# Kernel tuning notes

Measured on AMD Instinct MI355X. Metric: run time of the kernel, lower is better.

Reference implementation:

```python
import jax, jax.numpy as jnp
import numpy as np

DIM = 1024
NUM_HEADS = 16
HD = DIM // NUM_HEADS  # 64
ROPE_DIM = 64
ROPE_BASE = 10000.0


def setup_inputs() -> dict:
    key = jax.random.key(0)
    ks = jax.random.split(key, 5)
    B, N = 2, 2048
    s = 0.02
    return {
        "x": jax.random.normal(ks[0], (B, N, DIM), dtype=jnp.float32),
        "qkv_w": jax.random.normal(ks[1], (3 * DIM, DIM), dtype=jnp.float32) * s,
        "qkv_b": jax.random.normal(ks[2], (3 * DIM,), dtype=jnp.float32) * s,
        "proj_w": jax.random.normal(ks[3], (DIM, DIM), dtype=jnp.float32) * s,
        "proj_b": jax.random.normal(ks[4], (DIM,), dtype=jnp.float32) * s,
    }


def _apply_rope(t):
    # t: [B, H, N, D] with D even; interleaved (even, odd) pair rotation
    D = t.shape[-1]
    N = t.shape[2]
    pos = jnp.arange(N, dtype=t.dtype)
    inv = 1.0 / (ROPE_BASE ** (jnp.arange(0, D, 2, dtype=t.dtype) / D))
    freqs = pos[:, None] * inv[None, :]          # [N, D/2]
    cos = jnp.cos(freqs)[None, None]             # [1,1,N,D/2]
    sin = jnp.sin(freqs)[None, None]
    e = t[..., 0::2]
    o = t[..., 1::2]
    eo = e * cos - o * sin
    oo = e * sin + o * cos
    return jnp.stack([eo, oo], axis=-1).reshape(t.shape)


def reference(x, qkv_w, qkv_b, proj_w, proj_b):
    B, N, C = x.shape
    H, D = NUM_HEADS, HD
    scale = D ** -0.5
    qkv = x @ qkv_w.T + qkv_b                     # [B,N,3C]
    qkv = qkv.reshape(B, N, 3, H, D).transpose(2, 0, 3, 1, 4)  # [3,B,H,N,D]
    q, k, v = qkv[0], qkv[1], qkv[2]
    # RoPE on first ROPE_DIM dims of each head (here ROPE_DIM == HD)
    q = jnp.concatenate([_apply_rope(q[..., :ROPE_DIM]), q[..., ROPE_DIM:]], axis=-1)
    k = jnp.concatenate([_apply_rope(k[..., :ROPE_DIM]), k[..., ROPE_DIM:]], axis=-1)
    attn = jnp.einsum('bhnd,bhmd->bhnm', q, k) * scale
    attn = jax.nn.softmax(attn, axis=-1)
    out = jnp.einsum('bhnm,bhmd->bhnd', attn, v)  # [B,H,N,D]
    out = out.transpose(0, 2, 1, 3).reshape(B, N, C)
    return out @ proj_w.T + proj_b
```

## Files before the change

### kernel.cpp

```cpp
#include <hip/hip_runtime.h>
#include <hip/hip_bf16.h>
#include <stdint.h>

#define DIM   1024
#define NH    16
#define HDIM  64
#define SEQ   2048
#define BATCH 2
#define BHN   32
#define MTOK  4096
#define SC2   0.18033688f

using u16 = unsigned short;
using u32 = unsigned int;
typedef __attribute__((ext_vector_type(8))) short short8;
typedef __attribute__((ext_vector_type(4))) float f32x4;
typedef __attribute__((ext_vector_type(16))) float f32x16;

__device__ __forceinline__ u16 f2bf(float f) {
  __hip_bfloat16 h = __float2bfloat16(f);
  return *reinterpret_cast<u16*>(&h);
}
__device__ __forceinline__ u32 pk2(float lo, float hi) {
  return (u32)f2bf(lo) | ((u32)f2bf(hi) << 16);
}
__device__ __forceinline__ u32 cvtpk(float lo, float hi) {
  u32 r;
  asm("v_cvt_pk_bf16_f32 %0, %1, %2" : "=v"(r) : "v"(lo), "v"(hi));
  return r;
}
__device__ __forceinline__ float vexp2(float x) {
  float r;
  asm("v_exp_f32 %0, %1" : "=v"(r) : "v"(x));
  return r;
}

__device__ __forceinline__ void gload16(const void* g, void* lds) {
  __builtin_amdgcn_global_load_lds(
      (const __attribute__((address_space(1))) u32*)g,
      (__attribute__((address_space(3))) u32*)lds, 16, 0, 0);
}

#define PREP_A 1048576
#define PREP_B 1835008
#define PREP_C 2097152
#define PREP_E 2162688
__global__ void k_prep(const float4* __restrict__ x, const float4* __restrict__ qw,
                       const float4* __restrict__ pw, ushort4* __restrict__ xb,
                       ushort4* __restrict__ qwb, ushort4* __restrict__ pwb,
                       float2* __restrict__ tab) {
  int i = blockIdx.x * blockDim.x + threadIdx.x;
  if (i < PREP_A) {
    float4 v = x[i];
    xb[i] = make_ushort4(f2bf(v.x), f2bf(v.y), f2bf(v.z), f2bf(v.w));
  } else if (i < PREP_B) {
    int j = i - PREP_A;
    float4 v = qw[j];
    qwb[j] = make_ushort4(f2bf(v.x), f2bf(v.y), f2bf(v.z), f2bf(v.w));
  } else if (i < PREP_C) {
    int j = i - PREP_B;
    float4 v = pw[j];
    pwb[j] = make_ushort4(f2bf(v.x), f2bf(v.y), f2bf(v.z), f2bf(v.w));
  } else if (i < PREP_E) {
    int j = i - PREP_C;
    int n = j >> 5, f = j & 31;
    float inv = powf(10000.f, -(2.f * f) / 64.f);
    float s, c;
    sincosf((float)n * inv, &s, &c);
    tab[j] = make_float2(c, s);
  }
}

template <int EPI>
__global__ __launch_bounds__(256, 2) void k_gemm(
    const u16* __restrict__ A, const u16* __restrict__ Bt,
    const float* __restrict__ bias, int K,
    float* __restrict__ out_f, u16* __restrict__ qb, u16* __restrict__ kb,
    u16* __restrict__ vtb, const float2* __restrict__ tab) {
  __shared__ u16 As[128 * 64];
  __shared__ u16 Bs[128 * 64];
  const int tid = threadIdx.x;
  const int wid = tid >> 6, lane = tid & 63;
  const int lq = lane & 15, g = lane >> 4;
  const int wr = wid >> 1, wc = wid & 1;
  const int brow = blockIdx.y * 128;
  const int bcol = blockIdx.x * 128;
  f32x4 acc[4][4] = {};
  const u16* Ab = A + (size_t)brow * K;
  const u16* Bb = Bt + (size_t)bcol * K;

  for (int k0 = 0; k0 < K; k0 += 64) {
#pragma unroll
    for (int t = 0; t < 4; t++) {
      int rl = wid * 32 + t * 8 + (lane >> 3);
      int cs = (lane & 7) ^ (rl & 7);
      gload16(Ab + (size_t)rl * K + k0 + cs * 8, &As[(wid * 32 + t * 8) * 64]);
      gload16(Bb + (size_t)rl * K + k0 + cs * 8, &Bs[(wid * 32 + t * 8) * 64]);
    }
    __syncthreads();
#pragma unroll
    for (int kc = 0; kc < 2; kc++) {
      short8 af[4], bfr[4];
#pragma unroll
      for (int mt = 0; mt < 4; mt++) {
        int r = wr * 64 + mt * 16 + lq;
        af[mt] = *reinterpret_cast<const short8*>(&As[r * 64 + (((kc * 4 + g) ^ (r & 7)) * 8)]);
      }
#pragma unroll
      for (int nt = 0; nt < 4; nt++) {
        int r = wc * 64 + nt * 16 + lq;
        bfr[nt] = *reinterpret_cast<const short8*>(&Bs[r * 64 + (((kc * 4 + g) ^ (r & 7)) * 8)]);
      }
#pragma unroll
      for (int mt = 0; mt < 4; mt++)
#pragma unroll
        for (int nt = 0; nt < 4; nt++)
          acc[mt][nt] = __builtin_amdgcn_mfma_f32_16x16x32_bf16(af[mt], bfr[nt], acc[mt][nt], 0, 0, 0);
    }
    __syncthreads();
  }

#pragma unroll
  for (int mt = 0; mt < 4; mt++) {
    int row0 = brow + wr * 64 + mt * 16 + g * 4;
#pragma unroll
    for (int nt = 0; nt < 4; nt++) {
      int col = bcol + wc * 64 + nt * 16 + lq;
      float bv = bias[col];
      float v0 = acc[mt][nt][0] + bv;
      float v1 = acc[mt][nt][1] + bv;
      float v2 = acc[mt][nt][2] + bv;
      float v3 = acc[mt][nt][3] + bv;

      if (EPI == 1) {
        int which = col >> 10;
        if (which == 2) {
          int hd = col & 1023, d = hd & 63;
          int bb = row0 >> 11, n0 = row0 & 2047;
          int bh = bb * NH + (hd >> 6);
          uint2 pv = make_uint2(pk2(v0, v1), pk2(v2, v3));
          size_t idx = ((((size_t)bh * 32 + (n0 >> 6)) * 8 + ((n0 >> 3) & 7)) * 64 + d) * 8 + (n0 & 7);
          *reinterpret_cast<uint2*>(&vtb[idx]) = pv;
          continue;
        }
      }

      { float u = (lane & 1) ? v0 : v1; float s = __shfl_xor(u, 1); if (lane & 1) v0 = s; else v1 = s; }
      { float u = (lane & 1) ? v2 : v3; float s = __shfl_xor(u, 1); if (lane & 1) v2 = s; else v3 = s; }
      { float u = (lane & 2) ? v0 : v2; float s = __shfl_xor(u, 2); if (lane & 2) v0 = s; else v2 = s; }
      { float u = (lane & 2) ? v1 : v3; float s = __shfl_xor(u, 2); if (lane & 2) v1 = s; else v3 = s; }
      const int rr = row0 + (lane & 3);
      const int f0 = col & ~3;

      if (EPI == 0) {
        *reinterpret_cast<float4*>(&out_f[(size_t)rr * DIM + f0]) = make_float4(v0, v1, v2, v3);
      } else {
        int which = f0 >> 10, hd = f0 & 1023, hdh = hd >> 6, d0 = hd & 63;
        int bb = rr >> 11, n = rr & 2047;
        int bh = bb * NH + hdh;
        float2 cs0 = tab[n * 32 + (d0 >> 1)];
        float2 cs1 = tab[n * 32 + (d0 >> 1) + 1];
        float e0 = fmaf(-v1, cs0.y, v0 * cs0.x);
        float o0 = fmaf( v0, cs0.y, v1 * cs0.x);
        float e1 = fmaf(-v3, cs1.y, v2 * cs1.x);
        float o1 = fmaf( v2, cs1.y, v3 * cs1.x);
        if (which == 0) {
          uint2 pv = make_uint2(pk2(e0 * SC2, o0 * SC2), pk2(e1 * SC2, o1 * SC2));
          *reinterpret_cast<uint2*>(&qb[((size_t)bh * SEQ + n) * HDIM + d0]) = pv;
        } else {
          size_t idx = ((((size_t)bh * 32 + (n >> 6)) * 8 + (d0 >> 3)) * 64 + (n & 63)) * 8 + (d0 & 7);
          *reinterpret_cast<uint2*>(&kb[idx]) = make_uint2(pk2(e0, o0), pk2(e1, o1));
        }
      }
    }
  }
}

__global__ __launch_bounds__(256) void k_attn(
    const u16* __restrict__ qg, const u16* __restrict__ kg,
    const u16* __restrict__ vg, u16* __restrict__ aout) {
  __shared__ __align__(16) char smem[65536];
  const int tid = threadIdx.x;
  const int wid = tid >> 6, lane = tid & 63;
  const int l31 = lane & 31, h = lane >> 5;

  const int bid = blockIdx.x;
  const int xcd = bid & 7, slot = bid >> 3;
  const int bh = xcd * 4 + (slot >> 4);
  const int qt = slot & 15;
  const int b = bh >> 4, hh = bh & 15;
  const int q0 = qt * 128 + wid * 32;

  const u16* kbase = kg + (size_t)bh * SEQ * HDIM;
  const u16* vbase = vg + (size_t)bh * SEQ * HDIM;

  const u16* qrow = qg + ((size_t)bh * SEQ + q0 + l31) * HDIM;
  short8 qf[4];
#pragma unroll
  for (int c = 0; c < 4; c++)
    qf[c] = *reinterpret_cast<const short8*>(qrow + c * 16 + h * 8);

  short8 ones;
#pragma unroll
  for (int i = 0; i < 8; i++) ones[i] = (short)0x3F80;

  int koff[4];
#pragma unroll
  for (int c = 0; c < 4; c++)
    koff[c] = (2 * c + h) * 1024 + l31 * 16;

  f32x16 sA0, sA1, sB0, sB1;
  f32x16 oA = {}, oB = {}, ls = {};

  auto stage = [&](int buf, int tidx) {
    char* kd = smem + buf * 16384;
    const u16* kt = kbase + (size_t)tidx * 4096 + lane * 8;
    const u16* vt = vbase + (size_t)tidx * 4096 + lane * 8;
#pragma unroll
    for (int i = 0; i < 2; i++) {
      int g = wid + i * 4;
      gload16(kt + g * 512, kd + g * 1024);
      gload16(vt + g * 512, kd + 8192 + g * 1024);
    }
  };

  const int NT = SEQ / 64;

  auto body = [&](f32x16& sc0, f32x16& sc1, f32x16& sn0, f32x16& sn1, int t, bool last) {
    if (!last) asm volatile("s_waitcnt vmcnt(4)" ::: "memory");
    else       asm volatile("s_waitcnt vmcnt(0)" ::: "memory");
    __builtin_amdgcn_s_barrier();

    const char* kbp = smem + (t & 3) * 16384;
    const char* vbp = smem + ((t - 1) & 3) * 16384 + 8192;

#pragma unroll
    for (int c = 0; c < 4; c++) {
      short8 kf0 = *reinterpret_cast<const short8*>(kbp + koff[c]);
      short8 kf1 = *reinterpret_cast<const short8*>(kbp + koff[c] + 512);
      __builtin_amdgcn_s_setprio(1);
      if (c == 0) {
        f32x16 z = {};
        sn0 = __builtin_amdgcn_mfma_f32_32x32x16_bf16(kf0, qf[0], z, 0, 0, 0);
        sn1 = __builtin_amdgcn_mfma_f32_32x32x16_bf16(kf1, qf[0], z, 0, 0, 0);
      } else {
        sn0 = __builtin_amdgcn_mfma_f32_32x32x16_bf16(kf0, qf[c], sn0, 0, 0, 0);
        sn1 = __builtin_amdgcn_mfma_f32_32x32x16_bf16(kf1, qf[c], sn1, 0, 0, 0);
      }
      __builtin_amdgcn_s_setprio(0);

      if (c == 0 && t + 2 < NT) stage((t + 2) & 3, t + 2);

      short8 vf0 = *reinterpret_cast<const short8*>(vbp + koff[c]);
      short8 vf1 = *reinterpret_cast<const short8*>(vbp + koff[c] + 512);

      f32x16& sv = (c < 2) ? sc0 : sc1;
      const int e0 = (c & 1) * 8;
      float e[8];
#pragma unroll
      for (int j = 0; j < 8; j++) e[j] = vexp2(sv[e0 + j]);
      u32 a0 = cvtpk(e[0], e[1]), a1 = cvtpk(e[2], e[3]);
      u32 b0 = cvtpk(e[4], e[5]), b1 = cvtpk(e[6], e[7]);
      auto r0 = __builtin_amdgcn_permlane32_swap(a0, b0, false, false);
      auto r1 = __builtin_amdgcn_permlane32_swap(a1, b1, false, false);
      union { u32 u[4]; short8 v; } pp;
      pp.u[0] = r0[0]; pp.u[1] = r1[0]; pp.u[2] = r0[1]; pp.u[3] = r1[1];
      short8 pf = pp.v;

      __builtin_amdgcn_s_setprio(1);
      oA = __builtin_amdgcn_mfma_f32_32x32x16_bf16(vf0,  pf, oA, 0, 0, 0);
      oB = __builtin_amdgcn_mfma_f32_32x32x16_bf16(vf1,  pf, oB, 0, 0, 0);
      ls = __builtin_amdgcn_mfma_f32_32x32x16_bf16(ones, pf, ls, 0, 0, 0);
      __builtin_amdgcn_s_setprio(0);
    }
  };

  stage(0, 0);
  stage(1, 1);
  asm volatile("s_waitcnt vmcnt(4)" ::: "memory");
  __builtin_amdgcn_s_barrier();
  {
    const char* kbp = smem;
    f32x16 z = {};
    sA0 = z; sA1 = z;
#pragma unroll
    for (int c = 0; c < 4; c++) {
      short8 kf0 = *reinterpret_cast<const short8*>(kbp + koff[c]);
      short8 kf1 = *reinterpret_cast<const short8*>(kbp + koff[c] + 512);
      __builtin_amdgcn_s_setprio(1);
      sA0 = __builtin_amdgcn_mfma_f32_32x32x16_bf16(kf0, qf[c], sA0, 0, 0, 0);
      sA1 = __builtin_amdgcn_mfma_f32_32x32x16_bf16(kf1, qf[c], sA1, 0, 0, 0);
      __builtin_amdgcn_s_setprio(0);
      if (c == 0) stage(2, 2);
    }
  }

#pragma unroll 1
  for (int i = 0; i < 15; i++) {
    body(sA0, sA1, sB0, sB1, 2 * i + 1, false);
    body(sB0, sB1, sA0, sA1, 2 * i + 2, false);
  }
  body(sA0, sA1, sB0, sB1, 31, true);

  {
    const char* vbp = smem + 3 * 16384 + 8192;
#pragma unroll
    for (int c = 0; c < 4; c++) {
      short8 vf0 = *reinterpret_cast<const short8*>(vbp + koff[c]);
      short8 vf1 = *reinterpret_cast<const short8*>(vbp + koff[c] + 512);
      f32x16& sv = (c < 2) ? sB0 : sB1;
      const int e0 = (c & 1) * 8;
      float e[8];
#pragma unroll
      for (int j = 0; j < 8; j++) e[j] = vexp2(sv[e0 + j]);
      u32 a0 = cvtpk(e[0], e[1]), a1 = cvtpk(e[2], e[3]);
      u32 b0 = cvtpk(e[4], e[5]), b1 = cvtpk(e[6], e[7]);
      auto r0 = __builtin_amdgcn_permlane32_swap(a0, b0, false, false);
      auto r1 = __builtin_amdgcn_permlane32_swap(a1, b1, false, false);
      union { u32 u[4]; short8 v; } pp;
      pp.u[0] = r0[0]; pp.u[1] = r1[0]; pp.u[2] = r0[1]; pp.u[3] = r1[1];
      short8 pf = pp.v;
      oA = __builtin_amdgcn_mfma_f32_32x32x16_bf16(vf0,  pf, oA, 0, 0, 0);
      oB = __builtin_amdgcn_mfma_f32_32x32x16_bf16(vf1,  pf, oB, 0, 0, 0);
      ls = __builtin_amdgcn_mfma_f32_32x32x16_bf16(ones, pf, ls, 0, 0, 0);
    }
  }

  float invl = 1.0f / ls[0];
  int n = q0 + l31;
  u16* op = aout + ((size_t)(b * SEQ + n)) * DIM + hh * HDIM;
#pragma unroll
  for (int g = 0; g < 4; g++) {
    u32 w0 = pk2(oA[4 * g] * invl, oA[4 * g + 1] * invl);
    u32 w1 = pk2(oA[4 * g + 2] * invl, oA[4 * g + 3] * invl);
    *reinterpret_cast<uint2*>(op + 8 * g + 4 * h) = make_uint2(w0, w1);
    u32 x0 = pk2(oB[4 * g] * invl, oB[4 * g + 1] * invl);
    u32 x1 = pk2(oB[4 * g + 2] * invl, oB[4 * g + 3] * invl);
    *reinterpret_cast<uint2*>(op + 32 + 8 * g + 4 * h) = make_uint2(x0, x1);
  }
}

extern "C" void kernel_launch(void* const* d_in, const int* in_sizes, int n_in,
                              void* d_out, int out_size, void* d_ws, size_t ws_size,
                              hipStream_t stream) {
  (void)in_sizes; (void)n_in; (void)out_size; (void)ws_size;
  const float* x      = (const float*)d_in[0];
  const float* qkv_w  = (const float*)d_in[1];
  const float* qkv_b  = (const float*)d_in[2];
  const float* proj_w = (const float*)d_in[3];
  const float* proj_b = (const float*)d_in[4];
  float* out = (float*)d_out;

  char* w = (char*)d_ws;
  u16* xb     = (u16*)w;  w += (size_t)MTOK * DIM * 2;
  u16* wqkvb  = (u16*)w;  w += (size_t)3 * DIM * DIM * 2;
  u16* wprojb = (u16*)w;  w += (size_t)DIM * DIM * 2;
  u16* qb     = (u16*)w;  w += (size_t)BHN * SEQ * HDIM * 2;
  u16* kb     = (u16*)w;  w += (size_t)BHN * SEQ * HDIM * 2;
  u16* vtb    = (u16*)w;  w += (size_t)BHN * SEQ * HDIM * 2;
  u16* aout   = (u16*)w;  w += (size_t)MTOK * DIM * 2;
  float2* tab = (float2*)w;

  k_prep<<<(PREP_E + 255) / 256, 256, 0, stream>>>(
      (const float4*)x, (const float4*)qkv_w, (const float4*)proj_w,
      (ushort4*)xb, (ushort4*)wqkvb, (ushort4*)wprojb, tab);

  k_gemm<1><<<dim3(3 * DIM / 128, MTOK / 128), 256, 0, stream>>>(
      xb, wqkvb, qkv_b, DIM, nullptr, qb, kb, vtb, tab);

  k_attn<<<512, 256, 0, stream>>>(qb, kb, vtb, aout);

  k_gemm<0><<<dim3(DIM / 128, MTOK / 128), 256, 0, stream>>>(
      aout, wprojb, proj_b, DIM, out, nullptr, nullptr, nullptr, nullptr);
}
```

Baseline: 116.0 us.

## Double-buffer GEMM shared tiles with async prefetch two stages ahead

Result: slower. 124.0 us (+6.9%).

```diff
diff --git a/kernel.cpp b/kernel.cpp
--- a/kernel.cpp
+++ b/kernel.cpp
@@ -77,8 +77,8 @@
     const float* __restrict__ bias, int K,
     float* __restrict__ out_f, u16* __restrict__ qb, u16* __restrict__ kb,
     u16* __restrict__ vtb, const float2* __restrict__ tab) {
-  __shared__ u16 As[128 * 64];
-  __shared__ u16 Bs[128 * 64];
+  __shared__ u16 As[2][128 * 64];
+  __shared__ u16 Bs[2][128 * 64];
   const int tid = threadIdx.x;
   const int wid = tid >> 6, lane = tid & 63;
   const int lq = lane & 15, g = lane >> 4;
@@ -89,35 +89,53 @@
   const u16* Ab = A + (size_t)brow * K;
   const u16* Bb = Bt + (size_t)bcol * K;
 
-  for (int k0 = 0; k0 < K; k0 += 64) {
+  auto stage = [&](int buf, int k0) {
 #pragma unroll
     for (int t = 0; t < 4; t++) {
       int rl = wid * 32 + t * 8 + (lane >> 3);
       int cs = (lane & 7) ^ (rl & 7);
-      gload16(Ab + (size_t)rl * K + k0 + cs * 8, &As[(wid * 32 + t * 8) * 64]);
-      gload16(Bb + (size_t)rl * K + k0 + cs * 8, &Bs[(wid * 32 + t * 8) * 64]);
-    }
-    __syncthreads();
+      gload16(Ab + (size_t)rl * K + k0 + cs * 8, &As[buf][(wid * 32 + t * 8) * 64]);
+      gload16(Bb + (size_t)rl * K + k0 + cs * 8, &Bs[buf][(wid * 32 + t * 8) * 64]);
+    }
+  };
+
+  const int NS = K >> 6;
+  stage(0, 0);
+  stage(1, 64);
+
+#pragma unroll 1
+  for (int t = 0; t < NS; ++t) {
+    if (t < NS - 1) asm volatile("s_waitcnt vmcnt(8)" ::: "memory");
+    else            asm volatile("s_waitcnt vmcnt(0)" ::: "memory");
+    __builtin_amdgcn_s_barrier();
+
+    const u16* Ap = As[t & 1];
+    const u16* Bp = Bs[t & 1];
 #pragma unroll
     for (int kc = 0; kc < 2; kc++) {
       short8 af[4], bfr[4];
 #pragma unroll
       for (int mt = 0; mt < 4; mt++) {
         int r = wr * 64 + mt * 16 + lq;
-        af[mt] = *reinterpret_cast<const short8*>(&As[r * 64 + (((kc * 4 + g) ^ (r & 7)) * 8)]);
+        af[mt] = *reinterpret_cast<const short8*>(&Ap[r * 64 + (((kc * 4 + g) ^ (r & 7)) * 8)]);
       }
 #pragma unroll
       for (int nt = 0; nt < 4; nt++) {
         int r = wc * 64 + nt * 16 + lq;
-        bfr[nt] = *reinterpret_cast<const short8*>(&Bs[r * 64 + (((kc * 4 + g) ^ (r & 7)) * 8)]);
-      }
+        bfr[nt] = *reinterpret_cast<const short8*>(&Bp[r * 64 + (((kc * 4 + g) ^ (r & 7)) * 8)]);
+      }
+      __builtin_amdgcn_s_setprio(1);
 #pragma unroll
       for (int mt = 0; mt < 4; mt++)
 #pragma unroll
         for (int nt = 0; nt < 4; nt++)
           acc[mt][nt] = __builtin_amdgcn_mfma_f32_16x16x32_bf16(af[mt], bfr[nt], acc[mt][nt], 0, 0, 0);
-    }
-    __syncthreads();
+      __builtin_amdgcn_s_setprio(0);
+    }
+
+    asm volatile("s_waitcnt lgkmcnt(0)" ::: "memory");
+    __builtin_amdgcn_s_barrier();
+    if (t + 2 < NS) stage(t & 1, (t + 2) * 64);
   }
 
 #pragma unroll
```
